# Optimization experiments

Hardware: AMD Instinct MI355X
Metric: run time of the kernel (lower is better)

Reference implementation:

```python
import jax, jax.numpy as jnp
import numpy as np

EPS = 1e-8
C_RGLRU = 8.0  # Griffin constant

def rmsnorm(x, w):
    rms = jnp.sqrt(jnp.mean(x * x, axis=-1, keepdims=True) + EPS)
    return w * (x / rms)

def causal_depthwise_conv(x, conv_w, conv_b):
    # x: [B,S,H], conv_w: [K,H] depthwise causal conv, left-padded
    K = conv_w.shape[0]
    S = x.shape[1]
    xp = jnp.pad(x, ((0, 0), (K - 1, 0), (0, 0)))
    y = sum(conv_w[k] * xp[:, k:k + S, :] for k in range(K))
    return y + conv_b

def rg_lru(x, ga_W, ga_b, gx_W, gx_b, a_param):
    # x: [B,S,H]. Griffin RG-LRU: h_t = a_t h_{t-1} + sqrt(1-a_t^2) (i_t * x_t)
    r = jax.nn.sigmoid(x @ ga_W + ga_b)          # recurrence gate
    i = jax.nn.sigmoid(x @ gx_W + gx_b)          # input gate
    log_a = -C_RGLRU * jax.nn.softplus(a_param) * r
    a = jnp.exp(log_a)
    mult = jnp.sqrt(-jnp.expm1(2.0 * log_a))     # sqrt(1 - a^2), stable
    b = mult * (i * x)
    def combine(c1, c2):
        a1, b1 = c1
        a2, b2 = c2
        return a1 * a2, a2 * b1 + b2
    _, h = jax.lax.associative_scan(combine, (a, b), axis=1)
    return h

def setup_inputs() -> dict:
    D, H, F, K, B, S = 2048, 2048, 6144, 4, 2, 2048
    key = jax.random.key(0)
    ks = jax.random.split(key, 16)
    def lin(k, fan_in, shape):
        return jax.random.normal(k, shape, jnp.float32) * (fan_in ** -0.5)
    return {
        "x": jax.random.normal(ks[0], (B, S, D), jnp.float32),
        "norm1_w": jnp.ones((D,), jnp.float32),
        "left_W": lin(ks[1], D, (D, H)), "left_b": jnp.zeros((H,), jnp.float32),
        "right_W": lin(ks[2], D, (D, H)), "right_b": jnp.zeros((H,), jnp.float32),
        "conv_w": lin(ks[3], K, (K, H)), "conv_b": jnp.zeros((H,), jnp.float32),
        "ga_W": lin(ks[4], H, (H, H)), "ga_b": jnp.zeros((H,), jnp.float32),
        "gx_W": lin(ks[5], H, (H, H)), "gx_b": jnp.zeros((H,), jnp.float32),
        "a_param": jax.random.uniform(ks[6], (H,), jnp.float32, 0.5, 3.0),
        "out_W": lin(ks[7], H, (H, D)), "out_b": jnp.zeros((D,), jnp.float32),
        "norm2_w": jnp.ones((D,), jnp.float32),
        "up1_W": lin(ks[8], D, (D, F)), "up1_b": jnp.zeros((F,), jnp.float32),
        "up2_W": lin(ks[9], D, (D, F)), "up2_b": jnp.zeros((F,), jnp.float32),
        "down_W": lin(ks[10], F, (F, D)), "down_b": jnp.zeros((D,), jnp.float32),
    }

def reference(x, norm1_w, left_W, left_b, right_W, right_b, conv_w, conv_b,
              ga_W, ga_b, gx_W, gx_b, a_param, out_W, out_b,
              norm2_w, up1_W, up1_b, up2_W, up2_b, down_W, down_b):
    gelu = lambda t: jax.nn.gelu(t, approximate=False)
    # recurrent sub-block (pre-norm residual)
    xn = rmsnorm(x, norm1_w)
    left = gelu(xn @ left_W + left_b)
    right = rg_lru(causal_depthwise_conv(xn @ right_W + right_b, conv_w, conv_b),
                   ga_W, ga_b, gx_W, gx_b, a_param)
    x1 = (left * right) @ out_W + out_b + x
    # gated MLP sub-block (pre-norm residual)
    x1n = rmsnorm(x1, norm2_w)
    mlp = (gelu(x1n @ up1_W + up1_b) * (x1n @ up2_W + up2_b)) @ down_W + down_b
    return mlp + x1
```

## Files before the change

### kernel.cpp

```cpp
#include <hip/hip_runtime.h>
#include <cstdint>
#include <cstdio>

typedef __bf16 bf16x8 __attribute__((ext_vector_type(8)));
typedef float  f32x4  __attribute__((ext_vector_type(4)));
typedef const __attribute__((address_space(1))) void* gas_ptr;
typedef __attribute__((address_space(3))) void* las_ptr;

__device__ __forceinline__ uint16_t f32_to_bf16_rne(float f){
  uint32_t u = __builtin_bit_cast(uint32_t, f);
  u += 0x7FFFu + ((u >> 16) & 1u);
  return (uint16_t)(u >> 16);
}
__device__ __forceinline__ float bf16_to_f32(uint16_t h){
  uint32_t u = (uint32_t)h << 16;
  return __builtin_bit_cast(float, u);
}
__device__ __forceinline__ float gelu_exact(float x){
  return 0.5f * x * (1.f + erff(x * 0.7071067811865475f));
}

template<int EPI>
__device__ __forceinline__ void epi_store(float v, size_t idx, int row, int col,
    int N, int SPLIT, const float* auxF, const uint16_t* auxB,
    float* Cf, uint16_t* Cb0, uint16_t* Cb1, bool second)
{
  if constexpr (EPI == 1) {
    if (!second) Cb0[(size_t)row * SPLIT + col] = f32_to_bf16_rne(gelu_exact(v));
    else         Cb1[(size_t)row * (N - SPLIT) + (col - SPLIT)] = f32_to_bf16_rne(v);
  }
  if constexpr (EPI == 2) Cb0[idx] = f32_to_bf16_rne(v);
  if constexpr (EPI == 4) Cb0[idx] = f32_to_bf16_rne(v + auxF[idx]);
  if constexpr (EPI == 5) Cf[idx] = v + bf16_to_f32(auxB[idx]);
}

template<int EPI, int BM>
__global__ __launch_bounds__(512)
void gemm8p(const uint16_t* __restrict__ A, const uint16_t* __restrict__ Bt,
            const float* __restrict__ bias0, const float* __restrict__ bias1,
            const float* __restrict__ auxF, const uint16_t* __restrict__ auxB,
            float* __restrict__ Cf, uint16_t* __restrict__ Cb0, uint16_t* __restrict__ Cb1,
            int M, int N, int K, int SPLIT)
{
  constexpr int BN = 256;
  constexpr int M_REP   = BM / 32;
  constexpr int MH      = M_REP / 2;
  constexpr int LOADS_A = BM / 64;
  constexpr int LOADS_B = BN / 64;
  constexpr int LTOT    = LOADS_A + LOADS_B;
  constexpr int ASIZE   = BM * 128;
  constexpr int ABYTES  = 2 * ASIZE;
  constexpr int BSIZE   = BN * 128;
  __shared__ alignas(16) char smem[2 * (BM + BN) * 128];

  const int tid = threadIdx.x, lane = tid & 63, wid = tid >> 6;
  const int wm = wid >> 2, wn = wid & 3;
  const int la = lane & 15, lq = lane >> 4;
  const int n0 = blockIdx.x * BN, m0 = blockIdx.y * BM;

  const int rt = tid >> 3;
  const int gs = (tid & 7) ^ (rt & 7);
  const uint16_t* srcA = A  + (size_t)(m0 + rt) * K + gs * 8;
  const uint16_t* srcB = Bt + (size_t)(n0 + rt) * K + gs * 8;

  const int rowAb = (wm * (BM / 2) + la) * 128;
  const int rowBb = (wn * 64 + la) * 128;
  const int ck0 = ((lq)     ^ (la & 7)) * 16;
  const int ck1 = ((4 + lq) ^ (la & 7)) * 16;

  f32x4 acc[M_REP][4];
  const f32x4 fz = {0.f, 0.f, 0.f, 0.f};
#pragma unroll
  for (int m = 0; m < M_REP; ++m)
#pragma unroll
    for (int n = 0; n < 4; ++n) acc[m][n] = fz;

  bf16x8 aF[MH][2], bF0[2][2], bF1[2][2];
  const int NT = K >> 6;

#define STAGE_A8(KT, BUF) do { _Pragma("unroll")                              \
    for (int l = 0; l < LOADS_A; ++l)                                         \
      __builtin_amdgcn_global_load_lds(                                       \
          (gas_ptr)(srcA + (size_t)(KT) * 64 + (size_t)l * 64 * K),           \
          (las_ptr)(smem + (BUF) * ASIZE + (l * 512 + tid) * 16), 16, 0, 0);  \
  } while (0)
#define STAGE_B8(KT, BUF) do { _Pragma("unroll")                              \
    for (int l = 0; l < LOADS_B; ++l)                                         \
      __builtin_amdgcn_global_load_lds(                                       \
          (gas_ptr)(srcB + (size_t)(KT) * 64 + (size_t)l * 64 * K),           \
          (las_ptr)(smem + ABYTES + (BUF) * BSIZE + (l * 512 + tid) * 16),    \
          16, 0, 0);                                                          \
  } while (0)
#define RD_B8(DST, NH, BUF) do { _Pragma("unroll")                            \
    for (int nq = 0; nq < 2; ++nq) {                                          \
      int ro_ = ABYTES + (BUF) * BSIZE + rowBb + ((NH) * 2 + nq) * 2048;      \
      DST[nq][0] = *(const bf16x8*)(smem + ro_ + ck0);                        \
      DST[nq][1] = *(const bf16x8*)(smem + ro_ + ck1);                        \
    }                                                                         \
  } while (0)
#define RD_A8(MHS, BUF) do { _Pragma("unroll")                                \
    for (int mq = 0; mq < MH; ++mq) {                                         \
      int ro_ = (BUF) * ASIZE + rowAb + ((MHS) * MH + mq) * 2048;             \
      aF[mq][0] = *(const bf16x8*)(smem + ro_ + ck0);                         \
      aF[mq][1] = *(const bf16x8*)(smem + ro_ + ck1);                         \
    }                                                                         \
  } while (0)
#define MM8(MHS, NH, BF) do { _Pragma("unroll")                               \
    for (int mq = 0; mq < MH; ++mq)                                           \
      _Pragma("unroll")                                                       \
      for (int nq = 0; nq < 2; ++nq) {                                        \
        acc[(MHS)*MH+mq][(NH)*2+nq] = __builtin_amdgcn_mfma_f32_16x16x32_bf16(\
            aF[mq][0], BF[nq][0], acc[(MHS)*MH+mq][(NH)*2+nq], 0, 0, 0);      \
        acc[(MHS)*MH+mq][(NH)*2+nq] = __builtin_amdgcn_mfma_f32_16x16x32_bf16(\
            aF[mq][1], BF[nq][1], acc[(MHS)*MH+mq][(NH)*2+nq], 0, 0, 0);      \
      }                                                                       \
  } while (0)
#define BARR() __builtin_amdgcn_s_barrier()

  STAGE_A8(0, 0); STAGE_B8(0, 0);
  STAGE_A8(1, 1); STAGE_B8(1, 1);
  asm volatile("s_waitcnt vmcnt(%0)" :: "i"(LTOT) : "memory");
  BARR();

  for (int t = 0; t < NT; ++t) {
    const int buf = t & 1;
    const bool pf = (t + 2 < NT);
    RD_B8(bF0, 0, buf); RD_A8(0, buf);
    BARR();
    __builtin_amdgcn_s_setprio(1); MM8(0, 0, bF0); __builtin_amdgcn_s_setprio(0);
    BARR();
    RD_B8(bF1, 1, buf);
    BARR();
    __builtin_amdgcn_s_setprio(1); MM8(0, 1, bF1); __builtin_amdgcn_s_setprio(0);
    BARR();
    RD_A8(1, buf);
    if (pf) STAGE_B8(t + 2, buf);
    BARR();
    __builtin_amdgcn_s_setprio(1); MM8(1, 0, bF0); __builtin_amdgcn_s_setprio(0);
    BARR();
    if (pf) STAGE_A8(t + 2, buf);
    BARR();
    __builtin_amdgcn_s_setprio(1); MM8(1, 1, bF1); __builtin_amdgcn_s_setprio(0);
    if (pf) asm volatile("s_waitcnt vmcnt(%0)" :: "i"(LTOT) : "memory");
    else    asm volatile("s_waitcnt vmcnt(0)" ::: "memory");
    BARR();
  }
#undef STAGE_A8
#undef STAGE_B8
#undef RD_B8
#undef RD_A8
#undef MM8
#undef BARR

  if constexpr (EPI == 6) {
    const int GN = N >> 1;
#pragma unroll
    for (int np = 0; np < 2; ++np) {
      int gcol = (n0 >> 1) + wn * 32 + np * 16 + la;
      float b1 = bias0[gcol], b2 = bias1[gcol];
#pragma unroll
      for (int m = 0; m < M_REP; ++m) {
        int rbase = m0 + wm * (BM / 2) + m * 16 + lq * 4;
#pragma unroll
        for (int r = 0; r < 4; ++r) {
          int row = rbase + r;
          float v1 = acc[m][2*np][r] + b1;
          float v2 = acc[m][2*np+1][r] + b2;
          Cb0[(size_t)row * GN + gcol] = f32_to_bf16_rne(gelu_exact(v1) * v2);
        }
      }
    }
  } else {
#pragma unroll
    for (int n = 0; n < 4; ++n) {
      int col = n0 + wn * 64 + n * 16 + la;
      const bool second = (col >= SPLIT);
      float bv = second ? bias1[col - SPLIT] : bias0[col];
#pragma unroll
      for (int m = 0; m < M_REP; ++m) {
        int rbase = m0 + wm * (BM / 2) + m * 16 + lq * 4;
#pragma unroll
        for (int r = 0; r < 4; ++r) {
          int row = rbase + r;
          size_t idx = (size_t)row * N + col;
          epi_store<EPI>(acc[m][n][r] + bv, idx, row, col, N, SPLIT, auxF, auxB, Cf, Cb0, Cb1, second);
        }
      }
    }
  }
}

template<int EPI, int BM>
__global__ __launch_bounds__(512)
void gemm3b(const uint16_t* __restrict__ A, const uint16_t* __restrict__ Bt,
            const float* __restrict__ bias0, const float* __restrict__ bias1,
            const float* __restrict__ auxF, const uint16_t* __restrict__ auxB,
            float* __restrict__ Cf, uint16_t* __restrict__ Cb0, uint16_t* __restrict__ Cb1,
            int M, int N, int K, int SPLIT)
{
  constexpr int BN = 256;
  constexpr int M_REP   = BM / 32;
  constexpr int LOADS_A = BM / 64;
  constexpr int LOADS_B = BN / 64;
  constexpr int LTOT    = LOADS_A + LOADS_B;
  constexpr int BUFB    = (BM + BN) * 128;
  __shared__ alignas(16) char smem[3 * BUFB];

  const int tid  = threadIdx.x;
  const int lane = tid & 63;
  const int wid  = tid >> 6;
  const int wm = wid >> 2, wn = wid & 3;
  const int la = lane & 15, lq = lane >> 4;
  const int n0 = blockIdx.x * BN;
  const int m0 = blockIdx.y * BM;

  const int rt = tid >> 3;
  const int gs = (tid & 7) ^ (rt & 7);
  const uint16_t* srcA = A  + (size_t)(m0 + rt) * K + gs * 8;
  const uint16_t* srcB = Bt + (size_t)(n0 + rt) * K + gs * 8;

  const int rowAb = (wm * (BM / 2) + la) * 128;
  const int rowBb = BM * 128 + (wn * 64 + la) * 128;
  const int ck0 = ((lq)     ^ (la & 7)) * 16;
  const int ck1 = ((4 + lq) ^ (la & 7)) * 16;

  f32x4 acc[M_REP][4];
  const f32x4 fz = {0.f, 0.f, 0.f, 0.f};
#pragma unroll
  for (int m = 0; m < M_REP; ++m)
#pragma unroll
    for (int n = 0; n < 4; ++n) acc[m][n] = fz;

  const int NT = K >> 6;

#define STAGE3(KT, BUF) do {                                                  \
    const uint16_t* sa_ = srcA + (size_t)(KT) * 64;                           \
    const uint16_t* sb_ = srcB + (size_t)(KT) * 64;                           \
    char* base_ = smem + (BUF) * BUFB;                                        \
    _Pragma("unroll")                                                         \
    for (int l = 0; l < LOADS_A; ++l)                                         \
      __builtin_amdgcn_global_load_lds((gas_ptr)(sa_ + (size_t)l * 64 * K),   \
          (las_ptr)(base_ + (l * 512 + tid) * 16), 16, 0, 0);                 \
    _Pragma("unroll")                                                         \
    for (int l = 0; l < LOADS_B; ++l)                                         \
      __builtin_amdgcn_global_load_lds((gas_ptr)(sb_ + (size_t)l * 64 * K),   \
          (las_ptr)(base_ + BM * 128 + (l * 512 + tid) * 16), 16, 0, 0);      \
  } while (0)

  STAGE3(0, 0);
  STAGE3(1, 1);
  asm volatile("s_waitcnt vmcnt(%0)" :: "i"(LTOT) : "memory");
  __builtin_amdgcn_s_barrier();

  int cur = 0;
  for (int t = 0; t < NT; ++t) {
    const bool pf = (t + 2 < NT);
    if (pf) {
      int nxt = cur + 2; if (nxt >= 3) nxt -= 3;
      STAGE3(t + 2, nxt);
    }
    const char* base = smem + cur * BUFB;

    bf16x8 bF[4][2];
#pragma unroll
    for (int n = 0; n < 4; ++n) {
      const char* ro = base + rowBb + n * 2048;
      bF[n][0] = *(const bf16x8*)(ro + ck0);
      bF[n][1] = *(const bf16x8*)(ro + ck1);
    }
    __builtin_amdgcn_s_setprio(1);
#pragma unroll
    for (int m = 0; m < M_REP; ++m) {
      const char* ro = base + rowAb + m * 2048;
      bf16x8 a0 = *(const bf16x8*)(ro + ck0);
      bf16x8 a1 = *(const bf16x8*)(ro + ck1);
#pragma unroll
      for (int n = 0; n < 4; ++n) {
        acc[m][n] = __builtin_amdgcn_mfma_f32_16x16x32_bf16(a0, bF[n][0], acc[m][n], 0, 0, 0);
        acc[m][n] = __builtin_amdgcn_mfma_f32_16x16x32_bf16(a1, bF[n][1], acc[m][n], 0, 0, 0);
      }
    }
    __builtin_amdgcn_s_setprio(0);

    if (t + 1 < NT) {
      if (pf) asm volatile("s_waitcnt vmcnt(%0)" :: "i"(LTOT) : "memory");
      else    asm volatile("s_waitcnt vmcnt(0)" ::: "memory");
      __builtin_amdgcn_s_barrier();
      cur += 1; if (cur >= 3) cur -= 3;
    }
  }
#undef STAGE3

#pragma unroll
  for (int n = 0; n < 4; ++n) {
    int col = n0 + wn * 64 + n * 16 + la;
    const bool second = (col >= SPLIT);
    float bv = second ? bias1[col - SPLIT] : bias0[col];
#pragma unroll
    for (int m = 0; m < M_REP; ++m) {
      int rbase = m0 + wm * (BM / 2) + m * 16 + lq * 4;
#pragma unroll
      for (int r = 0; r < 4; ++r) {
        int row = rbase + r;
        size_t idx = (size_t)row * N + col;
        epi_store<EPI>(acc[m][n][r] + bv, idx, row, col, N, SPLIT, auxF, auxB, Cf, Cb0, Cb1, second);
      }
    }
  }
}

__global__ __launch_bounds__(256)
void cvt_transpose(const float* __restrict__ in, uint16_t* __restrict__ out, int R, int C)
{
  __shared__ float tile[64][65];
  const int r0 = blockIdx.y * 64, c0 = blockIdx.x * 64;
  const int t = threadIdx.x;
  const int lc = (t & 15) * 4;
  const int lr0 = t >> 4;
#pragma unroll
  for (int j = 0; j < 4; j++){
    int lr = lr0 + j*16;
    float4 v = *(const float4*)(in + (size_t)(r0 + lr) * C + c0 + lc);
    tile[lr][lc+0] = v.x; tile[lr][lc+1] = v.y; tile[lr][lc+2] = v.z; tile[lr][lc+3] = v.w;
  }
  __syncthreads();
  const int oc = t >> 2;
  const int rseg = (t & 3) * 16;
  alignas(16) uint16_t tmp[16];
#pragma unroll
  for (int j = 0; j < 16; j++) tmp[j] = f32_to_bf16_rne(tile[rseg + j][oc]);
  uint4* dst = (uint4*)(out + (size_t)(c0 + oc) * R + r0 + rseg);
  dst[0] = *(const uint4*)(&tmp[0]);
  dst[1] = *(const uint4*)(&tmp[8]);
}

__global__ __launch_bounds__(256)
void cvt_transpose_ileave(const float* __restrict__ in, uint16_t* __restrict__ out,
                          int R, int C, int half)
{
  __shared__ float tile[64][65];
  const int r0 = blockIdx.y * 64, c0 = blockIdx.x * 64;
  const int t = threadIdx.x;
  const int lc = (t & 15) * 4;
  const int lr0 = t >> 4;
#pragma unroll
  for (int j = 0; j < 4; j++){
    int lr = lr0 + j*16;
    float4 v = *(const float4*)(in + (size_t)(r0 + lr) * C + c0 + lc);
    tile[lr][lc+0] = v.x; tile[lr][lc+1] = v.y; tile[lr][lc+2] = v.z; tile[lr][lc+3] = v.w;
  }
  __syncthreads();
  const int oc = t >> 2;
  const int rseg = (t & 3) * 16;
  const int c = c0 + oc;
  const int wrow = ((c >> 4) << 5) + half * 16 + (c & 15);
  alignas(16) uint16_t tmp[16];
#pragma unroll
  for (int j = 0; j < 16; j++) tmp[j] = f32_to_bf16_rne(tile[rseg + j][oc]);
  uint4* dst = (uint4*)(out + (size_t)wrow * R + r0 + rseg);
  dst[0] = *(const uint4*)(&tmp[0]);
  dst[1] = *(const uint4*)(&tmp[8]);
}

__global__ __launch_bounds__(256)
void rmsnorm_kernel(const float* __restrict__ x, const float* __restrict__ w,
                    uint16_t* __restrict__ out, int D)
{
  const int row = blockIdx.x;
  const float* xr = x + (size_t)row * D;
  const int base = threadIdx.x * 8;
  float4 va = *(const float4*)(xr + base);
  float4 vb = *(const float4*)(xr + base + 4);
  float ss = va.x*va.x + va.y*va.y + va.z*va.z + va.w*va.w
           + vb.x*vb.x + vb.y*vb.y + vb.z*vb.z + vb.w*vb.w;
#pragma unroll
  for (int o = 32; o > 0; o >>= 1) ss += __shfl_xor(ss, o);
  __shared__ float red[4];
  if ((threadIdx.x & 63) == 0) red[threadIdx.x >> 6] = ss;
  __syncthreads();
  float tot = red[0] + red[1] + red[2] + red[3];
  float inv = rsqrtf(tot / (float)D + 1e-8f);
  float4 wa = *(const float4*)(w + base);
  float4 wb = *(const float4*)(w + base + 4);
  alignas(16) uint16_t tmp[8];
  tmp[0] = f32_to_bf16_rne(va.x * wa.x * inv);
  tmp[1] = f32_to_bf16_rne(va.y * wa.y * inv);
  tmp[2] = f32_to_bf16_rne(va.z * wa.z * inv);
  tmp[3] = f32_to_bf16_rne(va.w * wa.w * inv);
  tmp[4] = f32_to_bf16_rne(vb.x * wb.x * inv);
  tmp[5] = f32_to_bf16_rne(vb.y * wb.y * inv);
  tmp[6] = f32_to_bf16_rne(vb.z * wb.z * inv);
  tmp[7] = f32_to_bf16_rne(vb.w * wb.w * inv);
  *(uint4*)(out + (size_t)row * D + base) = *(const uint4*)tmp;
}

__global__ __launch_bounds__(256)
void rmsnorm_bf16_kernel(const uint16_t* __restrict__ x, const float* __restrict__ w,
                         uint16_t* __restrict__ out, int D)
{
  const int row = blockIdx.x;
  const uint16_t* xr = x + (size_t)row * D;
  const int base = threadIdx.x * 8;
  uint4 v = *(const uint4*)(xr + base);
  const uint16_t* vp = (const uint16_t*)&v;
  float xs[8];
  float ss = 0.f;
#pragma unroll
  for (int j = 0; j < 8; ++j){ xs[j] = bf16_to_f32(vp[j]); ss += xs[j]*xs[j]; }
#pragma unroll
  for (int o = 32; o > 0; o >>= 1) ss += __shfl_xor(ss, o);
  __shared__ float red[4];
  if ((threadIdx.x & 63) == 0) red[threadIdx.x >> 6] = ss;
  __syncthreads();
  float tot = red[0] + red[1] + red[2] + red[3];
  float inv = rsqrtf(tot / (float)D + 1e-8f);
  float4 wa = *(const float4*)(w + base);
  float4 wb = *(const float4*)(w + base + 4);
  float wv[8] = {wa.x, wa.y, wa.z, wa.w, wb.x, wb.y, wb.z, wb.w};
  alignas(16) uint16_t tmp[8];
#pragma unroll
  for (int j = 0; j < 8; ++j) tmp[j] = f32_to_bf16_rne(xs[j] * wv[j] * inv);
  *(uint4*)(out + (size_t)row * D + base) = *(const uint4*)tmp;
}

__global__ __launch_bounds__(256)
void conv_kernel(const uint16_t* __restrict__ xin, const float* __restrict__ cw,
                 const float* __restrict__ cb, uint16_t* __restrict__ yout,
                 int S, int H)
{
  const int h = blockIdx.x * 256 + threadIdx.x;
  const int b = blockIdx.z;
  const int t0 = blockIdx.y * 128;
  const float w0 = cw[h], w1 = cw[H + h], w2 = cw[2*H + h], w3 = cw[3*H + h];
  const float bias = cb[h];
  const size_t colbase = (size_t)b * S * H + h;
  float xm3 = (t0 >= 3) ? bf16_to_f32(xin[colbase + (size_t)(t0-3)*H]) : 0.f;
  float xm2 = (t0 >= 2) ? bf16_to_f32(xin[colbase + (size_t)(t0-2)*H]) : 0.f;
  float xm1 = (t0 >= 1) ? bf16_to_f32(xin[colbase + (size_t)(t0-1)*H]) : 0.f;
  for (int t = t0; t < t0 + 128; ++t){
    size_t idx = colbase + (size_t)t * H;
    float xt = bf16_to_f32(xin[idx]);
    float y = w0*xm3 + w1*xm2 + w2*xm1 + w3*xt + bias;
    yout[idx] = f32_to_bf16_rne(y);
    xm3 = xm2; xm2 = xm1; xm1 = xt;
  }
}

__device__ __forceinline__ void rglru_ab(float rp, float ip, float xc, float coef,
                                         float& a, float& bb)
{
  float r  = 1.f / (1.f + expf(-rp));
  float la = coef * r;
  a = expf(la);
  float mult = sqrtf(-expm1f(2.f * la));
  float ig = 1.f / (1.f + expf(-ip));
  bb = mult * ig * xc;
}

__global__ __launch_bounds__(256)
void scan_phase1(const uint16_t* __restrict__ gpre, const uint16_t* __restrict__ convb,
                 const float* __restrict__ ap,
                 float* __restrict__ SA, float* __restrict__ SB,
                 int S, int H, int T0, int NC)
{
  const int h = blockIdx.x * 256 + threadIdx.x;
  const int j = blockIdx.y, b = blockIdx.z;
  const float coef = -8.f * log1pf(expf(ap[h]));
  size_t rowb = (size_t)b * S + (size_t)j * T0;
  float A = 1.f, Bc = 0.f;
  for (int t = 0; t < T0; ++t){
    size_t row = rowb + t;
    float rp = bf16_to_f32(gpre[row * 2 * H + h]);
    float ip = bf16_to_f32(gpre[row * 2 * H + H + h]);
    float xc = bf16_to_f32(convb[row * H + h]);
    float a, bb; rglru_ab(rp, ip, xc, coef, a, bb);
    A *= a; Bc = a * Bc + bb;
  }
  size_t o = ((size_t)b * NC + j) * H + h;
  SA[o] = A; SB[o] = Bc;
}

__global__ __launch_bounds__(256)
void scan_phase2(const float* __restrict__ SA, const float* __restrict__ SB,
                 float* __restrict__ SH, int H, int NC)
{
  const int h = blockIdx.x * 256 + threadIdx.x;
  const int b = blockIdx.y;
  float hh = 0.f;
  for (int j = 0; j < NC; ++j){
    size_t o = ((size_t)b * NC + j) * H + h;
    SH[o] = hh;
    hh = SA[o] * hh + SB[o];
  }
}

__global__ __launch_bounds__(256)
void scan_phase3(const uint16_t* __restrict__ gpre, const uint16_t* __restrict__ convb,
                 const float* __restrict__ ap, const float* __restrict__ SH,
                 const uint16_t* __restrict__ left, uint16_t* __restrict__ lr,
                 int S, int H, int T0, int NC)
{
  const int h = blockIdx.x * 256 + threadIdx.x;
  const int j = blockIdx.y, b = blockIdx.z;
  const float coef = -8.f * log1pf(expf(ap[h]));
  float hh = SH[((size_t)b * NC + j) * H + h];
  size_t rowb = (size_t)b * S + (size_t)j * T0;
  for (int t = 0; t < T0; ++t){
    size_t row = rowb + t;
    float rp = bf16_to_f32(gpre[row * 2 * H + h]);
    float ip = bf16_to_f32(gpre[row * 2 * H + H + h]);
    float xc = bf16_to_f32(convb[row * H + h]);
    float a, bb; rglru_ab(rp, ip, xc, coef, a, bb);
    hh = a * hh + bb;
    lr[row * H + h] = f32_to_bf16_rne(bf16_to_f32(left[row * H + h]) * hh);
  }
}

extern "C" void kernel_launch(void* const* d_in, const int* in_sizes, int n_in,
                              void* d_out, int out_size, void* d_ws, size_t ws_size,
                              hipStream_t stream)
{
  const int B = 2, S = 2048, D = 2048, H = 2048, F = 6144;
  const int M = B * S;
  const int NC = 32, T0 = S / NC;

  const float* x       = (const float*)d_in[0];
  const float* norm1_w = (const float*)d_in[1];
  const float* left_W  = (const float*)d_in[2];
  const float* left_b  = (const float*)d_in[3];
  const float* right_W = (const float*)d_in[4];
  const float* right_b = (const float*)d_in[5];
  const float* conv_w  = (const float*)d_in[6];
  const float* conv_b  = (const float*)d_in[7];
  const float* ga_W    = (const float*)d_in[8];
  const float* ga_b    = (const float*)d_in[9];
  const float* gx_W    = (const float*)d_in[10];
  const float* gx_b    = (const float*)d_in[11];
  const float* a_param = (const float*)d_in[12];
  const float* out_W   = (const float*)d_in[13];
  const float* out_b   = (const float*)d_in[14];
  const float* norm2_w = (const float*)d_in[15];
  const float* up1_W   = (const float*)d_in[16];
  const float* up1_b   = (const float*)d_in[17];
  const float* up2_W   = (const float*)d_in[18];
  const float* up2_b   = (const float*)d_in[19];
  const float* down_W  = (const float*)d_in[20];
  const float* down_b  = (const float*)d_in[21];

  char* ws = (char*)d_ws;
  size_t off = 0;
  auto alloc = [&](size_t bytes) -> char* {
    char* p = ws + off; off += (bytes + 255) & ~(size_t)255; return p;
  };
  uint16_t* WT    = (uint16_t*)alloc((size_t)2 * F * D * 2);
  uint16_t* XN    = (uint16_t*)alloc((size_t)M * D * 2);
  uint16_t* LEFT  = (uint16_t*)alloc((size_t)M * H * 2);
  uint16_t* RPRE  = (uint16_t*)alloc((size_t)M * H * 2);
  uint16_t* CONVB = (uint16_t*)alloc((size_t)M * H * 2);
  uint16_t* GPRE  = (uint16_t*)alloc((size_t)M * 2 * H * 2);
  uint16_t* LR    = (uint16_t*)alloc((size_t)M * H * 2);
  uint16_t* X1B   = (uint16_t*)alloc((size_t)M * D * 2);
  uint16_t* X1N   = (uint16_t*)alloc((size_t)M * D * 2);
  float*    SA    = (float*)   alloc((size_t)B * NC * H * 4);
  float*    SB    = (float*)   alloc((size_t)B * NC * H * 4);
  float*    SHB   = (float*)   alloc((size_t)B * NC * H * 4);
  uint16_t* G     = XN;

  if (off > ws_size) {
    fprintf(stderr, "kernel_launch: ws too small, need %zu have %zu\n", off, ws_size);
    return;
  }

  float* OUT = (float*)d_out;
  dim3 blk(256);
  dim3 gblk(512);

  rmsnorm_kernel<<<M, blk, 0, stream>>>(x, norm1_w, XN, D);

  cvt_transpose<<<dim3(H/64, D/64), blk, 0, stream>>>(left_W, WT, D, H);
  cvt_transpose<<<dim3(H/64, D/64), blk, 0, stream>>>(right_W, WT + (size_t)H * D, D, H);
  gemm8p<1, 256><<<dim3((2*H)/256, M/256), gblk, 0, stream>>>(
      XN, WT, left_b, right_b, nullptr, nullptr, nullptr, LEFT, RPRE, M, 2*H, D, H);

  conv_kernel<<<dim3(H/256, S/128, B), blk, 0, stream>>>(RPRE, conv_w, conv_b, CONVB, S, H);

  cvt_transpose<<<dim3(H/64, H/64), blk, 0, stream>>>(ga_W, WT, H, H);
  cvt_transpose<<<dim3(H/64, H/64), blk, 0, stream>>>(gx_W, WT + (size_t)H * H, H, H);
  gemm8p<2, 256><<<dim3((2*H)/256, M/256), gblk, 0, stream>>>(
      CONVB, WT, ga_b, gx_b, nullptr, nullptr, nullptr, GPRE, nullptr, M, 2*H, H, H);

  scan_phase1<<<dim3(H/256, NC, B), blk, 0, stream>>>(GPRE, CONVB, a_param, SA, SB, S, H, T0, NC);
  scan_phase2<<<dim3(H/256, B), blk, 0, stream>>>(SA, SB, SHB, H, NC);
  scan_phase3<<<dim3(H/256, NC, B), blk, 0, stream>>>(GPRE, CONVB, a_param, SHB, LEFT, LR, S, H, T0, NC);

  cvt_transpose<<<dim3(D/64, H/64), blk, 0, stream>>>(out_W, WT, H, D);
  gemm3b<4, 128><<<dim3(D/256, M/128), gblk, 0, stream>>>(
      LR, WT, out_b, out_b, x, nullptr, nullptr, X1B, nullptr, M, D, H, D);

  rmsnorm_bf16_kernel<<<M, blk, 0, stream>>>(X1B, norm2_w, X1N, D);

  cvt_transpose_ileave<<<dim3(F/64, D/64), blk, 0, stream>>>(up1_W, WT, D, F, 0);
  cvt_transpose_ileave<<<dim3(F/64, D/64), blk, 0, stream>>>(up2_W, WT, D, F, 1);
  gemm8p<6, 256><<<dim3((2*F)/256, M/256), gblk, 0, stream>>>(
      X1N, WT, up1_b, up2_b, nullptr, nullptr, nullptr, G, nullptr, M, 2*F, D, 2*F);

  cvt_transpose<<<dim3(D/64, F/64), blk, 0, stream>>>(down_W, WT, F, D);
  gemm3b<5, 128><<<dim3(D/256, M/128), gblk, 0, stream>>>(
      G, WT, down_b, down_b, nullptr, X1B, OUT, nullptr, nullptr, M, D, F, D);
}
```

Baseline: 741.2 us.

## Switch narrow GEMMs to double-buffered LDS pipeline and add partial lgkm wait

The out-projection and down-projection GEMMs move from a three-buffer, prefetch-two-ahead pipeline to a two-buffer, prefetch-one-ahead pipeline, with A and B tiles held in separate LDS regions. The loop now waits for all outstanding global loads every iteration. The intent is to cut LDS footprint so more blocks fit per CU, at the cost of less latency hiding. The gemm8p kernel also gets an explicit partial lgkmcnt wait before its first barrier.

```diff
diff --git a/kernel.cpp b/kernel.cpp
--- a/kernel.cpp
+++ b/kernel.cpp
@@ -126,6 +126,7 @@
     const int buf = t & 1;
     const bool pf = (t + 2 < NT);
     RD_B8(bF0, 0, buf); RD_A8(0, buf);
+    asm volatile("s_waitcnt lgkmcnt(8)" ::: "memory");
     BARR();
     __builtin_amdgcn_s_setprio(1); MM8(0, 0, bF0); __builtin_amdgcn_s_setprio(0);
     BARR();
@@ -192,7 +193,7 @@
 
 template<int EPI, int BM>
 __global__ __launch_bounds__(512)
-void gemm3b(const uint16_t* __restrict__ A, const uint16_t* __restrict__ Bt,
+void gemm2p(const uint16_t* __restrict__ A, const uint16_t* __restrict__ Bt,
             const float* __restrict__ bias0, const float* __restrict__ bias1,
             const float* __restrict__ auxF, const uint16_t* __restrict__ auxB,
             float* __restrict__ Cf, uint16_t* __restrict__ Cb0, uint16_t* __restrict__ Cb1,
@@ -202,9 +203,8 @@
   constexpr int M_REP   = BM / 32;
   constexpr int LOADS_A = BM / 64;
   constexpr int LOADS_B = BN / 64;
-  constexpr int LTOT    = LOADS_A + LOADS_B;
-  constexpr int BUFB    = (BM + BN) * 128;
-  __shared__ alignas(16) char smem[3 * BUFB];
+  constexpr int ABYTES  = 2 * BM * 128;
+  __shared__ alignas(16) char smem[2 * (BM + BN) * 128];
 
   const int tid  = threadIdx.x;
   const int lane = tid & 63;
@@ -220,7 +220,7 @@
   const uint16_t* srcB = Bt + (size_t)(n0 + rt) * K + gs * 8;
 
   const int rowAb = (wm * (BM / 2) + la) * 128;
-  const int rowBb = BM * 128 + (wn * 64 + la) * 128;
+  const int rowBb = (wn * 64 + la) * 128;
   const int ck0 = ((lq)     ^ (la & 7)) * 16;
   const int ck1 = ((4 + lq) ^ (la & 7)) * 16;
 
@@ -233,47 +233,45 @@
 
   const int NT = K >> 6;
 
-#define STAGE3(KT, BUF) do {                                                  \
+#define STAGE(KT, BUF) do {                                                   \
     const uint16_t* sa_ = srcA + (size_t)(KT) * 64;                           \
     const uint16_t* sb_ = srcB + (size_t)(KT) * 64;                           \
-    char* base_ = smem + (BUF) * BUFB;                                        \
     _Pragma("unroll")                                                         \
     for (int l = 0; l < LOADS_A; ++l)                                         \
       __builtin_amdgcn_global_load_lds((gas_ptr)(sa_ + (size_t)l * 64 * K),   \
-          (las_ptr)(base_ + (l * 512 + tid) * 16), 16, 0, 0);                 \
+          (las_ptr)(smem + (BUF) * BM * 128 + (l * 512 + tid) * 16), 16, 0, 0);\
     _Pragma("unroll")                                                         \
     for (int l = 0; l < LOADS_B; ++l)                                         \
       __builtin_amdgcn_global_load_lds((gas_ptr)(sb_ + (size_t)l * 64 * K),   \
-          (las_ptr)(base_ + BM * 128 + (l * 512 + tid) * 16), 16, 0, 0);      \
+          (las_ptr)(smem + ABYTES + (BUF) * BN * 128 + (l * 512 + tid) * 16), \
+          16, 0, 0);                                                          \
   } while (0)
 
-  STAGE3(0, 0);
-  STAGE3(1, 1);
-  asm volatile("s_waitcnt vmcnt(%0)" :: "i"(LTOT) : "memory");
+  STAGE(0, 0);
+  asm volatile("s_waitcnt vmcnt(0)" ::: "memory");
   __builtin_amdgcn_s_barrier();
 
   int cur = 0;
-  for (int t = 0; t < NT; ++t) {
-    const bool pf = (t + 2 < NT);
-    if (pf) {
-      int nxt = cur + 2; if (nxt >= 3) nxt -= 3;
-      STAGE3(t + 2, nxt);
-    }
-    const char* base = smem + cur * BUFB;
+  for (int kt = 0; kt < NT; ++kt) {
+    const bool pf = (kt + 1 < NT);
+    if (pf) STAGE(kt + 1, cur ^ 1);
+
+    const int offA = cur * BM * 128;
+    const int offB = ABYTES + cur * BN * 128;
 
     bf16x8 bF[4][2];
 #pragma unroll
     for (int n = 0; n < 4; ++n) {
-      const char* ro = base + rowBb + n * 2048;
-      bF[n][0] = *(const bf16x8*)(ro + ck0);
-      bF[n][1] = *(const bf16x8*)(ro + ck1);
+      int ro = offB + rowBb + n * 2048;
+      bF[n][0] = *(const bf16x8*)(smem + ro + ck0);
+      bF[n][1] = *(const bf16x8*)(smem + ro + ck1);
     }
     __builtin_amdgcn_s_setprio(1);
 #pragma unroll
     for (int m = 0; m < M_REP; ++m) {
-      const char* ro = base + rowAb + m * 2048;
-      bf16x8 a0 = *(const bf16x8*)(ro + ck0);
-      bf16x8 a1 = *(const bf16x8*)(ro + ck1);
+      int ro = offA + rowAb + m * 2048;
+      bf16x8 a0 = *(const bf16x8*)(smem + ro + ck0);
+      bf16x8 a1 = *(const bf16x8*)(smem + ro + ck1);
 #pragma unroll
       for (int n = 0; n < 4; ++n) {
         acc[m][n] = __builtin_amdgcn_mfma_f32_16x16x32_bf16(a0, bF[n][0], acc[m][n], 0, 0, 0);
@@ -282,14 +280,13 @@
     }
     __builtin_amdgcn_s_setprio(0);
 
-    if (t + 1 < NT) {
-      if (pf) asm volatile("s_waitcnt vmcnt(%0)" :: "i"(LTOT) : "memory");
-      else    asm volatile("s_waitcnt vmcnt(0)" ::: "memory");
+    if (pf) {
+      asm volatile("s_waitcnt vmcnt(0)" ::: "memory");
       __builtin_amdgcn_s_barrier();
-      cur += 1; if (cur >= 3) cur -= 3;
+      cur ^= 1;
     }
   }
-#undef STAGE3
+#undef STAGE
 
 #pragma unroll
   for (int n = 0; n < 4; ++n) {
@@ -594,7 +591,7 @@
   scan_phase3<<<dim3(H/256, NC, B), blk, 0, stream>>>(GPRE, CONVB, a_param, SHB, LEFT, LR, S, H, T0, NC);
 
   cvt_transpose<<<dim3(D/64, H/64), blk, 0, stream>>>(out_W, WT, H, D);
-  gemm3b<4, 128><<<dim3(D/256, M/128), gblk, 0, stream>>>(
+  gemm2p<4, 128><<<dim3(D/256, M/128), gblk, 0, stream>>>(
       LR, WT, out_b, out_b, x, nullptr, nullptr, X1B, nullptr, M, D, H, D);
 
   rmsnorm_bf16_kernel<<<M, blk, 0, stream>>>(X1B, norm2_w, X1N, D);
@@ -605,6 +602,6 @@
       X1N, WT, up1_b, up2_b, nullptr, nullptr, nullptr, G, nullptr, M, 2*F, D, 2*F);
 
   cvt_transpose<<<dim3(D/64, F/64), blk, 0, stream>>>(down_W, WT, F, D);
-  gemm3b<5, 128><<<dim3(D/256, M/128), gblk, 0, stream>>>(
+  gemm2p<5, 128><<<dim3(D/256, M/128), gblk, 0, stream>>>(
       G, WT, down_b, down_b, nullptr, X1B, OUT, nullptr, nullptr, M, D, F, D);
 }
```

Measured after the change: 736.5 us, median of 2. Within noise of the previous version (-0.6%).
